# Kernel tuning notes

Hardware: AMD Instinct MI355X
Metric: run time of the kernel (lower is better)

## Reference

```python
import jax, jax.numpy as jnp
import numpy as np

B, N, OBS_DIM = 64, 512, 128
HIDDEN_DIM, MESSAGE_DIM, ACTION_DIM = 256, 128, 16


def _dense_params(key, din, dout):
    kw, kb = jax.random.split(key)
    W = jax.random.normal(kw, (din, dout), jnp.float32) * 0.02
    b = jnp.zeros((dout,), jnp.float32)
    return W, b


def setup_inputs() -> dict:
    key = jax.random.key(0)
    ks = jax.random.split(key, 12)
    obs_batch = jax.random.normal(ks[0], (B, N, OBS_DIM), jnp.float32)
    dones_batch = jnp.zeros((B, N), jnp.bool_)
    We, be = _dense_params(ks[1], OBS_DIM, HIDDEN_DIM)
    Wc, bc = _dense_params(ks[2], HIDDEN_DIM, MESSAGE_DIM // 4)
    Wn, bn = _dense_params(ks[3], HIDDEN_DIM, MESSAGE_DIM // 2)
    Wb, bb = _dense_params(ks[4], HIDDEN_DIM, MESSAGE_DIM // 4)
    Wi, bi = _dense_params(ks[5], HIDDEN_DIM, 1)
    Wq, bq = _dense_params(ks[6], HIDDEN_DIM, MESSAGE_DIM)
    Wk, bk = _dense_params(ks[7], MESSAGE_DIM, MESSAGE_DIM)
    Wv, bv = _dense_params(ks[8], MESSAGE_DIM, MESSAGE_DIM)
    Wp, bp = _dense_params(ks[9], HIDDEN_DIM + MESSAGE_DIM, HIDDEN_DIM)
    Wa, ba = _dense_params(ks[10], HIDDEN_DIM, ACTION_DIM)
    Wcr, bcr = _dense_params(ks[11], HIDDEN_DIM, 1)
    return {"obs_batch": obs_batch, "dones_batch": dones_batch,
            "We": We, "be": be, "Wc": Wc, "bc": bc, "Wn": Wn, "bn": bn,
            "Wb": Wb, "bb": bb, "Wi": Wi, "bi": bi, "Wq": Wq, "bq": bq,
            "Wk": Wk, "bk": bk, "Wv": Wv, "bv": bv, "Wp": Wp, "bp": bp,
            "Wa": Wa, "ba": ba, "Wcr": Wcr, "bcr": bcr}


def reference(obs_batch, dones_batch, We, be, Wc, bc, Wn, bn, Wb, bb, Wi, bi,
              Wq, bq, Wk, bk, Wv, bv, Wp, bp, Wa, ba, Wcr, bcr):
    dense = lambda x, W, b: x @ W + b
    encoded = jax.nn.relu(dense(obs_batch, We, be))                 # [B,N,H]
    messages = jnp.concatenate([dense(encoded, Wc, bc),
                                dense(encoded, Wn, bn),
                                dense(encoded, Wb, bb)], axis=-1)   # [B,N,M]
    importance = jax.nn.sigmoid(dense(encoded, Wi, bi))             # [B,N,1]
    Q = dense(encoded, Wq, bq)
    K = dense(messages, Wk, bk)
    V = dense(messages, Wv, bv)
    scores = jnp.einsum('bqd,bkd->bqk', Q, K) / jnp.sqrt(jnp.float32(MESSAGE_DIM))
    importance_weights = importance * jnp.transpose(importance, (0, 2, 1))  # [B,N,N]
    scores = scores * importance_weights
    norms = jnp.linalg.norm(obs_batch, axis=-1, keepdims=True)      # [B,N,1]
    obs_sim = jnp.einsum('bid,bjd->bij', obs_batch, obs_batch)
    obs_sim = obs_sim / (norms + 1e-08)
    obs_sim = obs_sim / (jnp.transpose(norms, (0, 2, 1)) + 1e-08)
    scores = scores + obs_sim * 0.5
    attn = jax.nn.softmax(scores, axis=-1)
    aggregated = jnp.einsum('bqk,bkd->bqd', attn, V)                # [B,N,M]
    combined = jnp.concatenate([encoded, aggregated], axis=-1)
    x = jax.nn.relu(dense(combined, Wp, bp))
    logits = dense(x, Wa, ba)
    value = dense(x, Wcr, bcr).squeeze(-1)
    return (logits, value)
```

## Files before the change

### kernel.cpp

```cpp
#include <hip/hip_runtime.h>
#include <math.h>


typedef __attribute__((ext_vector_type(8))) short short8;
typedef __attribute__((ext_vector_type(4))) float f32x4;

#define RSQRT_D 0.08838834764831843f

__device__ __forceinline__ unsigned short f2bf(float f) {
  union { float f; unsigned u; } v; v.f = f;
  return (unsigned short)((v.u + 0x7FFFu + ((v.u >> 16) & 1u)) >> 16);
}
__device__ __forceinline__ float bf2f(unsigned short h) {
  union { unsigned u; float f; } v; v.u = ((unsigned)h) << 16;
  return v.f;
}
__device__ __forceinline__ unsigned pack2(float a, float b) {
  return (unsigned)f2bf(a) | ((unsigned)f2bf(b) << 16);
}

__device__ __forceinline__ int swz(int row, int chunk) {
  return row * 128 + ((chunk ^ ((row & 7) << 1)) << 3);
}

__global__ __launch_bounds__(256) void prep_w(
    const float* __restrict__ We, const float* __restrict__ Wq,
    const float* __restrict__ Wk, const float* __restrict__ Wv,
    const float* __restrict__ Wp, const float* __restrict__ Wc,
    const float* __restrict__ Wn, const float* __restrict__ Wb,
    const float* __restrict__ bc, const float* __restrict__ bn,
    const float* __restrict__ bb, const float* __restrict__ Wa,
    const float* __restrict__ Wcr, unsigned short* __restrict__ WeT,
    unsigned short* __restrict__ Wmq, unsigned short* __restrict__ Wkv,
    unsigned short* __restrict__ WpT, unsigned short* __restrict__ WaCrT,
    float* __restrict__ bm) {
  int idx = blockIdx.x * 256 + threadIdx.x;
  if (idx < 32768) {
    int n = idx >> 7, k = idx & 127;
    WeT[idx] = f2bf(We[k * 256 + n]);
  } else if (idx < 65536) {
    int i = idx - 32768;
    int d = i >> 8, h = i & 255;
    float v = (d < 32)   ? Wc[h * 32 + d]
            : (d < 96)   ? Wn[h * 64 + (d - 32)]
                         : Wb[h * 32 + (d - 96)];
    Wmq[i] = f2bf(v);
  } else if (idx < 98304) {
    int i = idx - 65536;
    int n = i >> 8, k = i & 255;
    Wmq[32768 + i] = f2bf(Wq[k * 128 + n]);
  } else if (idx < 114688) {
    int i = idx - 98304;
    int n = i >> 7, k = i & 127;
    Wkv[i] = f2bf(Wk[k * 128 + n]);
  } else if (idx < 131072) {
    int i = idx - 114688;
    int n = i >> 7, k = i & 127;
    Wkv[16384 + i] = f2bf(Wv[k * 128 + n]);
  } else if (idx < 229376) {
    int i = idx - 131072;
    int n = i / 384, k = i - n * 384;
    WpT[i] = f2bf(Wp[k * 256 + n]);
  } else if (idx < 237568) {
    int i = idx - 229376;
    int n = i >> 8, k = i & 255;
    float v = (n < 16) ? Wa[k * 16 + n] : (n == 16) ? Wcr[k] : 0.f;
    WaCrT[i] = f2bf(v);
  } else if (idx < 237696) {
    int i = idx - 237568;
    bm[i] = (i < 32) ? bc[i] : (i < 96) ? bn[i - 32] : bb[i - 96];
  }
}

__global__ __launch_bounds__(256) void prep_obs(
    const float* __restrict__ obs, unsigned short* __restrict__ obs_bf,
    unsigned short* __restrict__ As, unsigned short* __restrict__ Bs) {
  int t = blockIdx.x * 4 + (threadIdx.x >> 6);
  int lane = threadIdx.x & 63;
  const float* row = obs + (size_t)t * 128;
  float2 o = *(const float2*)(row + lane * 2);
  float s2 = o.x * o.x + o.y * o.y;
#pragma unroll
  for (int off = 1; off < 64; off <<= 1) s2 += __shfl_xor(s2, off);
  float inv = 1.f / (sqrtf(s2) + 1e-8f);
  ((unsigned*)obs_bf)[(size_t)t * 64 + lane] = pack2(o.x, o.y);
  ((unsigned*)As)[(size_t)t * 128 + 64 + lane] =
      pack2(o.x * 0.5f * inv, o.y * 0.5f * inv);
  ((unsigned*)Bs)[(size_t)t * 128 + 64 + lane] = pack2(o.x * inv, o.y * inv);
}

__global__ __launch_bounds__(256) void imp_kernel(
    const unsigned short* __restrict__ enc, const float* __restrict__ Wi,
    const float* __restrict__ bi, float* __restrict__ impA,
    float* __restrict__ impB) {
  int t = blockIdx.x * 4 + (threadIdx.x >> 6);
  int lane = threadIdx.x & 63;
  const unsigned* eu = (const unsigned*)(enc + (size_t)t * 256);
  unsigned u0 = eu[lane * 2], u1 = eu[lane * 2 + 1];
  float4 w = *(const float4*)(Wi + lane * 4);
  float s = bf2f((unsigned short)(u0 & 0xFFFF)) * w.x +
            bf2f((unsigned short)(u0 >> 16)) * w.y +
            bf2f((unsigned short)(u1 & 0xFFFF)) * w.z +
            bf2f((unsigned short)(u1 >> 16)) * w.w;
#pragma unroll
  for (int off = 1; off < 64; off <<= 1) s += __shfl_xor(s, off);
  if (lane == 0) {
    float sg = 1.0f / (1.0f + __expf(-(s + bi[0])));
    impA[t] = sg * RSQRT_D;
    impB[t] = sg;
  }
}

template <int MODE>
__device__ __forceinline__ void epi_store(unsigned short* out, int ldc,
                                          const float* bias,
                                          const float* scale, int rowb,
                                          int col, const f32x4& a) {
  const float bv = bias ? bias[col] : 0.f;
  if constexpr (MODE == 3) {
    unsigned short t0 = f2bf(a[0] + bv), t1 = f2bf(a[1] + bv);
    unsigned short t2 = f2bf(a[2] + bv), t3 = f2bf(a[3] + bv);
    uint2 o;
    o.x = (unsigned)t0 | ((unsigned)t1 << 16);
    o.y = (unsigned)t2 | ((unsigned)t3 << 16);
    *(uint2*)(out + ((size_t)(rowb >> 9) * 128 + col) * 512 + (rowb & 511)) = o;
  } else {
#pragma unroll
    for (int r = 0; r < 4; ++r) {
      float v = a[r] + bv;
      if constexpr (MODE == 1) v = fmaxf(v, 0.f);
      if constexpr (MODE == 2) v *= scale[rowb + r];
      out[(size_t)(rowb + r) * ldc + col] = f2bf(v);
    }
  }
}

template <int M0, int M1>
__global__ __launch_bounds__(256, 2) void gemm_dual(
    const unsigned short* __restrict__ A1, int lda1, int K1,
    const unsigned short* __restrict__ A2, int lda2, int Ktot,
    const unsigned short* __restrict__ Bt, int ldb,
    const float* __restrict__ bias0, const float* __restrict__ bias1,
    const float* __restrict__ scale, unsigned short* __restrict__ out0,
    int ldc0, unsigned short* __restrict__ out1, int ldc1, int xsplit) {
  __shared__ unsigned short Asr[64][72];
  __shared__ unsigned short Bsr[128][72];
  const int tid = threadIdx.x;
  const int lane = tid & 63, wave = tid >> 6;
  const int quad = lane >> 4, l16 = lane & 15;
  const int wm = wave & 1, wn = wave >> 1;
  const int bm = blockIdx.y * 64, bn = blockIdx.x * 128;

  f32x4 acc[2][4];
#pragma unroll
  for (int i = 0; i < 2; ++i)
#pragma unroll
    for (int j = 0; j < 4; ++j) acc[i][j] = (f32x4){0.f, 0.f, 0.f, 0.f};

  const int ar = tid >> 3, ac = tid & 7;
  for (int kt = 0; kt < Ktot; kt += 64) {
    const unsigned short* Asrc;
    int lda, kloc;
    if (kt < K1) { Asrc = A1; lda = lda1; kloc = kt; }
    else         { Asrc = A2; lda = lda2; kloc = kt - K1; }
#pragma unroll
    for (int it = 0; it < 2; ++it) {
      int r = ar + it * 32;
      uint4 v = *(const uint4*)(Asrc + (size_t)(bm + r) * lda + kloc + ac * 8);
      *(uint4*)&Asr[r][ac * 8] = v;
    }
#pragma unroll
    for (int it = 0; it < 4; ++it) {
      int r = ar + it * 32;
      uint4 v = *(const uint4*)(Bt + (size_t)(bn + r) * ldb + kt + ac * 8);
      *(uint4*)&Bsr[r][ac * 8] = v;
    }
    __syncthreads();
#pragma unroll
    for (int ks = 0; ks < 64; ks += 32) {
      short8 af[2], bfr[4];
#pragma unroll
      for (int i = 0; i < 2; ++i)
        af[i] = *(const short8*)&Asr[wm * 32 + i * 16 + l16][ks + quad * 8];
#pragma unroll
      for (int j = 0; j < 4; ++j)
        bfr[j] = *(const short8*)&Bsr[wn * 64 + j * 16 + l16][ks + quad * 8];
#pragma unroll
      for (int i = 0; i < 2; ++i)
#pragma unroll
        for (int j = 0; j < 4; ++j)
          acc[i][j] = __builtin_amdgcn_mfma_f32_16x16x32_bf16(af[i], bfr[j],
                                                              acc[i][j], 0, 0, 0);
    }
    __syncthreads();
  }
  const int colb = bn + wn * 64 + l16;
#pragma unroll
  for (int i = 0; i < 2; ++i) {
    const int rowb = bm + wm * 32 + i * 16 + quad * 4;
#pragma unroll
    for (int j = 0; j < 4; ++j) {
      const int col = colb + j * 16;
      if (col < xsplit)
        epi_store<M0>(out0, ldc0, bias0, scale, rowb, col, acc[i][j]);
      else
        epi_store<M1>(out1, ldc1, bias1, scale, rowb, col - xsplit, acc[i][j]);
    }
  }
}

__global__ __launch_bounds__(256, 3) void flash2(
    const unsigned short* __restrict__ As, const unsigned short* __restrict__ Bs,
    const unsigned short* __restrict__ vT, unsigned short* __restrict__ agg) {
  __shared__ unsigned short Ub[128 * 128];
  __shared__ unsigned short Pp[32 * 128];
  __shared__ float redm[2][32];
  __shared__ float reds[2][32];
  const int tid = threadIdx.x;
  const int lane = tid & 63, wave = tid >> 6;
  const int quad = lane >> 4, l16 = lane & 15;
  const int wm = wave & 1, wn = wave >> 1;
  const int b = blockIdx.x & 63;
  const int qt = blockIdx.x >> 6;
  const size_t tokA = (size_t)b * 512 + qt * 32;

  short8 af[8];
#pragma unroll
  for (int kc = 0; kc < 8; ++kc)
    af[kc] = *(const short8*)(As + (tokA + wm * 16 + l16) * 256 + kc * 32 +
                              quad * 8);

  f32x4 s[4][4];
#pragma unroll
  for (int kt = 0; kt < 4; ++kt)
#pragma unroll
    for (int nt = 0; nt < 4; ++nt) s[kt][nt] = (f32x4){0.f, 0.f, 0.f, 0.f};

  const int lr = tid >> 4, lc = tid & 15;

#pragma unroll
  for (int kt = 0; kt < 4; ++kt) {
#pragma unroll
    for (int kh = 0; kh < 2; ++kh) {
      __syncthreads();
#pragma unroll
      for (int it = 0; it < 8; ++it) {
        int r = lr + it * 16;
        *(uint4*)&Ub[swz(r, lc)] =
            *(const uint4*)(Bs + ((size_t)b * 512 + kt * 128 + r) * 256 +
                            kh * 128 + lc * 8);
      }
      __syncthreads();
#pragma unroll
      for (int kk = 0; kk < 4; ++kk) {
        short8 bfr[4];
#pragma unroll
        for (int nt = 0; nt < 4; ++nt) {
          int rrow = wn * 64 + nt * 16 + l16;
          bfr[nt] = *(const short8*)&Ub[swz(rrow, kk * 4 + quad)];
        }
#pragma unroll
        for (int nt = 0; nt < 4; ++nt)
          s[kt][nt] = __builtin_amdgcn_mfma_f32_16x16x32_bf16(
              af[kh * 4 + kk], bfr[nt], s[kt][nt], 0, 0, 0);
      }
    }
  }

  const int rbase = wm * 16 + quad * 4;
  float mt4[4];
#pragma unroll
  for (int r = 0; r < 4; ++r) {
    float mv = -1e30f;
#pragma unroll
    for (int kt = 0; kt < 4; ++kt)
#pragma unroll
      for (int nt = 0; nt < 4; ++nt) mv = fmaxf(mv, s[kt][nt][r]);
#pragma unroll
    for (int off = 1; off < 16; off <<= 1) mv = fmaxf(mv, __shfl_xor(mv, off));
    mt4[r] = mv;
  }
  if (l16 == 0) {
#pragma unroll
    for (int r = 0; r < 4; ++r) redm[wn][rbase + r] = mt4[r];
  }
  __syncthreads();
  float lsum[4];
#pragma unroll
  for (int r = 0; r < 4; ++r) {
    float mfull = fmaxf(mt4[r], redm[1 ^ wn][rbase + r]);
    float sum = 0.f;
#pragma unroll
    for (int kt = 0; kt < 4; ++kt)
#pragma unroll
      for (int nt = 0; nt < 4; ++nt) {
        float p = __expf(s[kt][nt][r] - mfull);
        s[kt][nt][r] = p;
        sum += p;
      }
#pragma unroll
    for (int off = 1; off < 16; off <<= 1) sum += __shfl_xor(sum, off);
    lsum[r] = sum;
  }
  if (l16 == 0) {
#pragma unroll
    for (int r = 0; r < 4; ++r) reds[wn][rbase + r] = lsum[r];
  }
  __syncthreads();
  float linv[4];
#pragma unroll
  for (int r = 0; r < 4; ++r)
    linv[r] = 1.0f / (lsum[r] + reds[1 ^ wn][rbase + r]);

  f32x4 oacc[4];
#pragma unroll
  for (int nt = 0; nt < 4; ++nt) oacc[nt] = (f32x4){0.f, 0.f, 0.f, 0.f};
#pragma unroll
  for (int vt = 0; vt < 4; ++vt) {
    __syncthreads();
#pragma unroll
    for (int nt = 0; nt < 4; ++nt)
#pragma unroll
      for (int r = 0; r < 4; ++r) {
        int row = rbase + r;
        int col = wn * 64 + nt * 16 + l16;
        Pp[row * 128 + (((col >> 3) ^ ((row & 7) << 1)) << 3) + (col & 7)] =
            f2bf(s[vt][nt][r]);
      }
#pragma unroll
    for (int it = 0; it < 8; ++it) {
      int r = lr + it * 16;
      *(uint4*)&Ub[swz(r, lc)] =
          *(const uint4*)(vT + ((size_t)b * 128 + r) * 512 + vt * 128 + lc * 8);
    }
    __syncthreads();
#pragma unroll
    for (int kk = 0; kk < 4; ++kk) {
      short8 pa = *(const short8*)&Pp[swz(wm * 16 + l16, kk * 4 + quad)];
#pragma unroll
      for (int nt = 0; nt < 4; ++nt) {
        int rrow = wn * 64 + nt * 16 + l16;
        short8 vb = *(const short8*)&Ub[swz(rrow, kk * 4 + quad)];
        oacc[nt] = __builtin_amdgcn_mfma_f32_16x16x32_bf16(pa, vb, oacc[nt],
                                                           0, 0, 0);
      }
    }
  }

#pragma unroll
  for (int nt = 0; nt < 4; ++nt) {
    const int col = wn * 64 + nt * 16 + l16;
#pragma unroll
    for (int r = 0; r < 4; ++r)
      agg[(tokA + rbase + r) * 128 + col] = f2bf(oacc[nt][r] * linv[r]);
  }
}

__global__ __launch_bounds__(256, 3) void xh_gemm(
    const unsigned short* __restrict__ A1, const unsigned short* __restrict__ A2,
    const unsigned short* __restrict__ WpT, const float* __restrict__ bp,
    const unsigned short* __restrict__ WaCrT, const float* __restrict__ ba,
    const float* __restrict__ bcr, float* __restrict__ logits,
    float* __restrict__ value) {
  __shared__ unsigned short Asr[32][72];
  __shared__ unsigned short Bsr[256][72];
  const int tid = threadIdx.x;
  const int lane = tid & 63, wave = tid >> 6;
  const int quad = lane >> 4, l16 = lane & 15;
  const int bm = blockIdx.x * 32;

  f32x4 acc[2][4];
#pragma unroll
  for (int i = 0; i < 2; ++i)
#pragma unroll
    for (int j = 0; j < 4; ++j) acc[i][j] = (f32x4){0.f, 0.f, 0.f, 0.f};

  const int ar = tid >> 3, ac = tid & 7;
  for (int kt = 0; kt < 384; kt += 64) {
    const unsigned short* Asrc;
    int lda, kloc;
    if (kt < 256) { Asrc = A1; lda = 256; kloc = kt; }
    else          { Asrc = A2; lda = 128; kloc = kt - 256; }
    *(uint4*)&Asr[ar][ac * 8] =
        *(const uint4*)(Asrc + (size_t)(bm + ar) * lda + kloc + ac * 8);
#pragma unroll
    for (int it = 0; it < 8; ++it) {
      int idx = tid + it * 256;
      int r = idx >> 3, c = idx & 7;
      *(uint4*)&Bsr[r][c * 8] = *(const uint4*)(WpT + (size_t)r * 384 + kt + c * 8);
    }
    __syncthreads();
#pragma unroll
    for (int kk = 0; kk < 2; ++kk) {
      short8 afr[2], bfr[4];
#pragma unroll
      for (int i = 0; i < 2; ++i)
        afr[i] = *(const short8*)&Asr[i * 16 + l16][kk * 32 + quad * 8];
#pragma unroll
      for (int j = 0; j < 4; ++j)
        bfr[j] = *(const short8*)&Bsr[wave * 64 + j * 16 + l16][kk * 32 + quad * 8];
#pragma unroll
      for (int i = 0; i < 2; ++i)
#pragma unroll
        for (int j = 0; j < 4; ++j)
          acc[i][j] = __builtin_amdgcn_mfma_f32_16x16x32_bf16(afr[i], bfr[j],
                                                              acc[i][j], 0, 0, 0);
    }
    __syncthreads();
  }
  unsigned short* xs = &Bsr[0][0];
#pragma unroll
  for (int i = 0; i < 2; ++i) {
    const int row = i * 16 + quad * 4;
#pragma unroll
    for (int j = 0; j < 4; ++j) {
      const int col = wave * 64 + j * 16 + l16;
      const float bv = bp[col];
#pragma unroll
      for (int r = 0; r < 4; ++r)
        xs[(row + r) * 264 + col] = f2bf(fmaxf(acc[i][j][r] + bv, 0.f));
    }
  }
  __syncthreads();
  const int wm2 = wave & 1, wn2 = wave >> 1;
  f32x4 hacc = (f32x4){0.f, 0.f, 0.f, 0.f};
#pragma unroll
  for (int kk = 0; kk < 8; ++kk) {
    short8 pa = *(const short8*)&xs[(wm2 * 16 + l16) * 264 + kk * 32 + quad * 8];
    short8 wb = *(const short8*)(WaCrT + (size_t)(wn2 * 16 + l16) * 256 +
                                 kk * 32 + quad * 8);
    hacc = __builtin_amdgcn_mfma_f32_16x16x32_bf16(pa, wb, hacc, 0, 0, 0);
  }
  const int n = wn2 * 16 + l16;
#pragma unroll
  for (int r = 0; r < 4; ++r) {
    const size_t tok = bm + wm2 * 16 + quad * 4 + r;
    if (n < 16)
      logits[tok * 16 + n] = hacc[r] + ba[n];
    else if (n == 16)
      value[tok] = hacc[r] + bcr[0];
  }
}

extern "C" void kernel_launch(void* const* d_in, const int* in_sizes, int n_in,
                              void* d_out, int out_size, void* d_ws,
                              size_t ws_size, hipStream_t stream) {
  const float* obs = (const float*)d_in[0];
  const float* We = (const float*)d_in[2];
  const float* be = (const float*)d_in[3];
  const float* Wc = (const float*)d_in[4];
  const float* bc = (const float*)d_in[5];
  const float* Wn = (const float*)d_in[6];
  const float* bn = (const float*)d_in[7];
  const float* Wb = (const float*)d_in[8];
  const float* bb = (const float*)d_in[9];
  const float* Wi = (const float*)d_in[10];
  const float* bi = (const float*)d_in[11];
  const float* Wq = (const float*)d_in[12];
  const float* bq = (const float*)d_in[13];
  const float* Wk = (const float*)d_in[14];
  const float* bk = (const float*)d_in[15];
  const float* Wv = (const float*)d_in[16];
  const float* bv = (const float*)d_in[17];
  const float* Wp = (const float*)d_in[18];
  const float* bp = (const float*)d_in[19];
  const float* Wa = (const float*)d_in[20];
  const float* ba = (const float*)d_in[21];
  const float* Wcr = (const float*)d_in[22];
  const float* bcr = (const float*)d_in[23];

  char* base = (char*)d_ws;
  unsigned short* enc_bf = (unsigned short*)(base);
  unsigned short* As     = (unsigned short*)(base + 16777216);
  unsigned short* Bs     = (unsigned short*)(base + 33554432);
  unsigned short* obsagg = (unsigned short*)(base + 50331648);
  unsigned short* msg_bf = (unsigned short*)(base + 58720256);
  unsigned short* vT     = (unsigned short*)(base + 75497472);
  float* impA            = (float*)(base + 83886080);
  float* impB            = (float*)(base + 84017152);
  unsigned short* WeT    = (unsigned short*)(base + 84148224);
  unsigned short* Wmq    = (unsigned short*)(base + 84213760);
  unsigned short* Wkv    = (unsigned short*)(base + 84344832);
  unsigned short* WpT    = (unsigned short*)(base + 84410368);
  float* bmb             = (float*)(base + 84606976);
  unsigned short* WaCrT  = (unsigned short*)(base + 84607488);

  prep_w<<<929, 256, 0, stream>>>(We, Wq, Wk, Wv, Wp, Wc, Wn, Wb, bc, bn, bb,
                                  Wa, Wcr, WeT, Wmq, Wkv, WpT, WaCrT, bmb);
  prep_obs<<<8192, 256, 0, stream>>>(obs, obsagg, As, Bs);

  gemm_dual<1, 1><<<dim3(2, 512), 256, 0, stream>>>(
      obsagg, 128, 128, nullptr, 0, 128, WeT, 128, be, be, nullptr, enc_bf,
      256, enc_bf, 256, 256);
  imp_kernel<<<8192, 256, 0, stream>>>(enc_bf, Wi, bi, impA, impB);

  gemm_dual<0, 2><<<dim3(2, 512), 256, 0, stream>>>(
      enc_bf, 256, 256, nullptr, 0, 256, Wmq, 256, bmb, bq, impA, msg_bf, 128,
      As, 256, 128);
  gemm_dual<2, 3><<<dim3(2, 512), 256, 0, stream>>>(
      msg_bf, 128, 128, nullptr, 0, 128, Wkv, 128, bk, bv, impB, Bs, 256, vT,
      0, 128);

  flash2<<<1024, 256, 0, stream>>>(As, Bs, vT, obsagg);

  xh_gemm<<<1024, 256, 0, stream>>>(enc_bf, obsagg, WpT, bp, WaCrT, ba, bcr,
                                    (float*)d_out, (float*)d_out + 524288);
}
```

Baseline: 223.2 us.

## Replace LDS-staged GEMMs with direct-load MFMA kernels and fuse importance into encoder

Every GEMM kernel now loads MFMA fragments straight from global memory instead of staging tiles through shared memory with barriers. The importance projection and sigmoid move into the encoder GEMM epilogue, which removes a separate kernel and a re-read of the encoded activations. The attention kernel is restructured so each wave owns a 128-key slice, with a four-way cross-wave max and sum reduction and the whole P tile kept in LDS. The trade-off is more redundant global and L2 traffic from unshared fragment loads, and the loss of the LDS swizzling.

```diff
diff --git a/kernel.cpp b/kernel.cpp
--- a/kernel.cpp
+++ b/kernel.cpp
@@ -6,6 +6,7 @@
 typedef __attribute__((ext_vector_type(4))) float f32x4;
 
 #define RSQRT_D 0.08838834764831843f
+#define MFMA __builtin_amdgcn_mfma_f32_16x16x32_bf16
 
 __device__ __forceinline__ unsigned short f2bf(float f) {
   union { float f; unsigned u; } v; v.f = f;
@@ -18,9 +19,8 @@
 __device__ __forceinline__ unsigned pack2(float a, float b) {
   return (unsigned)f2bf(a) | ((unsigned)f2bf(b) << 16);
 }
-
-__device__ __forceinline__ int swz(int row, int chunk) {
-  return row * 128 + ((chunk ^ ((row & 7) << 1)) << 3);
+__device__ __forceinline__ short8 ld8(const unsigned short* p) {
+  return *(const short8*)p;
 }
 
 __global__ __launch_bounds__(256) void prep_w(
@@ -89,336 +89,351 @@
   ((unsigned*)Bs)[(size_t)t * 128 + 64 + lane] = pack2(o.x * inv, o.y * inv);
 }
 
-__global__ __launch_bounds__(256) void imp_kernel(
-    const unsigned short* __restrict__ enc, const float* __restrict__ Wi,
-    const float* __restrict__ bi, float* __restrict__ impA,
+__global__ __launch_bounds__(256) void enc_gemm(
+    const unsigned short* __restrict__ obs_bf,
+    const unsigned short* __restrict__ WeT, const float* __restrict__ be,
+    const float* __restrict__ Wi, const float* __restrict__ bi,
+    unsigned short* __restrict__ enc, float* __restrict__ impA,
     float* __restrict__ impB) {
-  int t = blockIdx.x * 4 + (threadIdx.x >> 6);
-  int lane = threadIdx.x & 63;
-  const unsigned* eu = (const unsigned*)(enc + (size_t)t * 256);
-  unsigned u0 = eu[lane * 2], u1 = eu[lane * 2 + 1];
-  float4 w = *(const float4*)(Wi + lane * 4);
-  float s = bf2f((unsigned short)(u0 & 0xFFFF)) * w.x +
-            bf2f((unsigned short)(u0 >> 16)) * w.y +
-            bf2f((unsigned short)(u1 & 0xFFFF)) * w.z +
-            bf2f((unsigned short)(u1 >> 16)) * w.w;
-#pragma unroll
-  for (int off = 1; off < 64; off <<= 1) s += __shfl_xor(s, off);
-  if (lane == 0) {
-    float sg = 1.0f / (1.0f + __expf(-(s + bi[0])));
-    impA[t] = sg * RSQRT_D;
-    impB[t] = sg;
-  }
-}
-
-template <int MODE>
-__device__ __forceinline__ void epi_store(unsigned short* out, int ldc,
-                                          const float* bias,
-                                          const float* scale, int rowb,
-                                          int col, const f32x4& a) {
-  const float bv = bias ? bias[col] : 0.f;
-  if constexpr (MODE == 3) {
-    unsigned short t0 = f2bf(a[0] + bv), t1 = f2bf(a[1] + bv);
-    unsigned short t2 = f2bf(a[2] + bv), t3 = f2bf(a[3] + bv);
-    uint2 o;
-    o.x = (unsigned)t0 | ((unsigned)t1 << 16);
-    o.y = (unsigned)t2 | ((unsigned)t3 << 16);
-    *(uint2*)(out + ((size_t)(rowb >> 9) * 128 + col) * 512 + (rowb & 511)) = o;
-  } else {
+  __shared__ float ired[4][32];
+  const int tid = threadIdx.x, lane = tid & 63, wave = tid >> 6;
+  const int quad = lane >> 4, l16 = lane & 15;
+  const int bm = blockIdx.x * 32;
+  f32x4 acc[2][4];
+#pragma unroll
+  for (int i = 0; i < 2; ++i)
+#pragma unroll
+    for (int j = 0; j < 4; ++j) acc[i][j] = (f32x4){0.f, 0.f, 0.f, 0.f};
+#pragma unroll
+  for (int kc = 0; kc < 4; ++kc) {
+    short8 af[2], bf[4];
+#pragma unroll
+    for (int i = 0; i < 2; ++i)
+      af[i] = ld8(obs_bf + (size_t)(bm + i * 16 + l16) * 128 + kc * 32 + quad * 8);
+#pragma unroll
+    for (int j = 0; j < 4; ++j)
+      bf[j] = ld8(WeT + (size_t)(wave * 64 + j * 16 + l16) * 128 + kc * 32 + quad * 8);
+#pragma unroll
+    for (int i = 0; i < 2; ++i)
+#pragma unroll
+      for (int j = 0; j < 4; ++j) acc[i][j] = MFMA(af[i], bf[j], acc[i][j], 0, 0, 0);
+  }
+  float ip[2][4];
+#pragma unroll
+  for (int i = 0; i < 2; ++i)
+#pragma unroll
+    for (int r = 0; r < 4; ++r) ip[i][r] = 0.f;
+#pragma unroll
+  for (int i = 0; i < 2; ++i)
+#pragma unroll
+    for (int j = 0; j < 4; ++j) {
+      const int col = wave * 64 + j * 16 + l16;
+      const float bv = be[col], wv = Wi[col];
+      const int rowb = bm + i * 16 + quad * 4;
+#pragma unroll
+      for (int r = 0; r < 4; ++r) {
+        float v = fmaxf(acc[i][j][r] + bv, 0.f);
+        enc[(size_t)(rowb + r) * 256 + col] = f2bf(v);
+        ip[i][r] += v * wv;
+      }
+    }
+#pragma unroll
+  for (int i = 0; i < 2; ++i)
 #pragma unroll
     for (int r = 0; r < 4; ++r) {
-      float v = a[r] + bv;
-      if constexpr (MODE == 1) v = fmaxf(v, 0.f);
-      if constexpr (MODE == 2) v *= scale[rowb + r];
-      out[(size_t)(rowb + r) * ldc + col] = f2bf(v);
-    }
-  }
-}
-
-template <int M0, int M1>
-__global__ __launch_bounds__(256, 2) void gemm_dual(
-    const unsigned short* __restrict__ A1, int lda1, int K1,
-    const unsigned short* __restrict__ A2, int lda2, int Ktot,
-    const unsigned short* __restrict__ Bt, int ldb,
-    const float* __restrict__ bias0, const float* __restrict__ bias1,
-    const float* __restrict__ scale, unsigned short* __restrict__ out0,
-    int ldc0, unsigned short* __restrict__ out1, int ldc1, int xsplit) {
-  __shared__ unsigned short Asr[64][72];
-  __shared__ unsigned short Bsr[128][72];
-  const int tid = threadIdx.x;
-  const int lane = tid & 63, wave = tid >> 6;
+#pragma unroll
+      for (int off = 1; off < 16; off <<= 1)
+        ip[i][r] += __shfl_xor(ip[i][r], off);
+    }
+  if (l16 == 0) {
+#pragma unroll
+    for (int i = 0; i < 2; ++i)
+#pragma unroll
+      for (int r = 0; r < 4; ++r)
+        ired[wave][i * 16 + quad * 4 + r] = ip[i][r];
+  }
+  __syncthreads();
+  if (tid < 32) {
+    float s = ired[0][tid] + ired[1][tid] + ired[2][tid] + ired[3][tid] + bi[0];
+    float sg = 1.0f / (1.0f + __expf(-s));
+    impA[bm + tid] = sg * RSQRT_D;
+    impB[bm + tid] = sg;
+  }
+}
+
+__global__ __launch_bounds__(256) void msgq_gemm(
+    const unsigned short* __restrict__ enc, const unsigned short* __restrict__ Wmq,
+    const float* __restrict__ bm, const float* __restrict__ bq,
+    const float* __restrict__ impA, unsigned short* __restrict__ msg,
+    unsigned short* __restrict__ As) {
+  const int tid = threadIdx.x, lane = tid & 63, wave = tid >> 6;
   const int quad = lane >> 4, l16 = lane & 15;
-  const int wm = wave & 1, wn = wave >> 1;
-  const int bm = blockIdx.y * 64, bn = blockIdx.x * 128;
-
+  const int bmr = blockIdx.x * 32;
   f32x4 acc[2][4];
 #pragma unroll
   for (int i = 0; i < 2; ++i)
 #pragma unroll
     for (int j = 0; j < 4; ++j) acc[i][j] = (f32x4){0.f, 0.f, 0.f, 0.f};
-
-  const int ar = tid >> 3, ac = tid & 7;
-  for (int kt = 0; kt < Ktot; kt += 64) {
-    const unsigned short* Asrc;
-    int lda, kloc;
-    if (kt < K1) { Asrc = A1; lda = lda1; kloc = kt; }
-    else         { Asrc = A2; lda = lda2; kloc = kt - K1; }
-#pragma unroll
-    for (int it = 0; it < 2; ++it) {
-      int r = ar + it * 32;
-      uint4 v = *(const uint4*)(Asrc + (size_t)(bm + r) * lda + kloc + ac * 8);
-      *(uint4*)&Asr[r][ac * 8] = v;
-    }
-#pragma unroll
-    for (int it = 0; it < 4; ++it) {
-      int r = ar + it * 32;
-      uint4 v = *(const uint4*)(Bt + (size_t)(bn + r) * ldb + kt + ac * 8);
-      *(uint4*)&Bsr[r][ac * 8] = v;
-    }
-    __syncthreads();
-#pragma unroll
-    for (int ks = 0; ks < 64; ks += 32) {
-      short8 af[2], bfr[4];
-#pragma unroll
-      for (int i = 0; i < 2; ++i)
-        af[i] = *(const short8*)&Asr[wm * 32 + i * 16 + l16][ks + quad * 8];
-#pragma unroll
-      for (int j = 0; j < 4; ++j)
-        bfr[j] = *(const short8*)&Bsr[wn * 64 + j * 16 + l16][ks + quad * 8];
-#pragma unroll
-      for (int i = 0; i < 2; ++i)
-#pragma unroll
-        for (int j = 0; j < 4; ++j)
-          acc[i][j] = __builtin_amdgcn_mfma_f32_16x16x32_bf16(af[i], bfr[j],
-                                                              acc[i][j], 0, 0, 0);
-    }
-    __syncthreads();
-  }
-  const int colb = bn + wn * 64 + l16;
+#pragma unroll
+  for (int kc = 0; kc < 8; ++kc) {
+    short8 af[2], bf[4];
+#pragma unroll
+    for (int i = 0; i < 2; ++i)
+      af[i] = ld8(enc + (size_t)(bmr + i * 16 + l16) * 256 + kc * 32 + quad * 8);
+#pragma unroll
+    for (int j = 0; j < 4; ++j)
+      bf[j] = ld8(Wmq + (size_t)(wave * 64 + j * 16 + l16) * 256 + kc * 32 + quad * 8);
+#pragma unroll
+    for (int i = 0; i < 2; ++i)
+#pragma unroll
+      for (int j = 0; j < 4; ++j) acc[i][j] = MFMA(af[i], bf[j], acc[i][j], 0, 0, 0);
+  }
 #pragma unroll
   for (int i = 0; i < 2; ++i) {
-    const int rowb = bm + wm * 32 + i * 16 + quad * 4;
+    const int rowb = bmr + i * 16 + quad * 4;
 #pragma unroll
     for (int j = 0; j < 4; ++j) {
-      const int col = colb + j * 16;
-      if (col < xsplit)
-        epi_store<M0>(out0, ldc0, bias0, scale, rowb, col, acc[i][j]);
-      else
-        epi_store<M1>(out1, ldc1, bias1, scale, rowb, col - xsplit, acc[i][j]);
-    }
-  }
-}
-
-__global__ __launch_bounds__(256, 3) void flash2(
+      const int col = wave * 64 + j * 16 + l16;
+      if (col < 128) {
+        const float bv = bm[col];
+#pragma unroll
+        for (int r = 0; r < 4; ++r)
+          msg[(size_t)(rowb + r) * 128 + col] = f2bf(acc[i][j][r] + bv);
+      } else {
+        const int c = col - 128;
+        const float bv = bq[c];
+#pragma unroll
+        for (int r = 0; r < 4; ++r)
+          As[(size_t)(rowb + r) * 256 + c] =
+              f2bf((acc[i][j][r] + bv) * impA[rowb + r]);
+      }
+    }
+  }
+}
+
+__global__ __launch_bounds__(256) void kv_gemm(
+    const unsigned short* __restrict__ msg, const unsigned short* __restrict__ Wkv,
+    const float* __restrict__ bk, const float* __restrict__ bv,
+    const float* __restrict__ impB, unsigned short* __restrict__ Bs,
+    unsigned short* __restrict__ vT) {
+  const int tid = threadIdx.x, lane = tid & 63, wave = tid >> 6;
+  const int quad = lane >> 4, l16 = lane & 15;
+  const int bmr = blockIdx.x * 32;
+  f32x4 acc[2][4];
+#pragma unroll
+  for (int i = 0; i < 2; ++i)
+#pragma unroll
+    for (int j = 0; j < 4; ++j) acc[i][j] = (f32x4){0.f, 0.f, 0.f, 0.f};
+#pragma unroll
+  for (int kc = 0; kc < 4; ++kc) {
+    short8 af[2], bf[4];
+#pragma unroll
+    for (int i = 0; i < 2; ++i)
+      af[i] = ld8(msg + (size_t)(bmr + i * 16 + l16) * 128 + kc * 32 + quad * 8);
+#pragma unroll
+    for (int j = 0; j < 4; ++j)
+      bf[j] = ld8(Wkv + (size_t)(wave * 64 + j * 16 + l16) * 128 + kc * 32 + quad * 8);
+#pragma unroll
+    for (int i = 0; i < 2; ++i)
+#pragma unroll
+      for (int j = 0; j < 4; ++j) acc[i][j] = MFMA(af[i], bf[j], acc[i][j], 0, 0, 0);
+  }
+#pragma unroll
+  for (int i = 0; i < 2; ++i) {
+    const int rowb = bmr + i * 16 + quad * 4;
+#pragma unroll
+    for (int j = 0; j < 4; ++j) {
+      const int col = wave * 64 + j * 16 + l16;
+      if (col < 128) {
+        const float bvv = bk[col];
+#pragma unroll
+        for (int r = 0; r < 4; ++r)
+          Bs[(size_t)(rowb + r) * 256 + col] =
+              f2bf((acc[i][j][r] + bvv) * impB[rowb + r]);
+      } else {
+        const int c = col - 128;
+        const float bvv = bv[c];
+        uint2 o;
+        o.x = pack2(acc[i][j][0] + bvv, acc[i][j][1] + bvv);
+        o.y = pack2(acc[i][j][2] + bvv, acc[i][j][3] + bvv);
+        *(uint2*)(vT + ((size_t)(rowb >> 9) * 128 + c) * 512 + (rowb & 511)) = o;
+      }
+    }
+  }
+}
+
+__global__ __launch_bounds__(256) void flash3(
     const unsigned short* __restrict__ As, const unsigned short* __restrict__ Bs,
     const unsigned short* __restrict__ vT, unsigned short* __restrict__ agg) {
-  __shared__ unsigned short Ub[128 * 128];
-  __shared__ unsigned short Pp[32 * 128];
-  __shared__ float redm[2][32];
-  __shared__ float reds[2][32];
-  const int tid = threadIdx.x;
-  const int lane = tid & 63, wave = tid >> 6;
+  __shared__ unsigned short Pp[32 * 520];
+  __shared__ float redm[4][32];
+  __shared__ float reds[4][32];
+  const int tid = threadIdx.x, lane = tid & 63, wave = tid >> 6;
   const int quad = lane >> 4, l16 = lane & 15;
-  const int wm = wave & 1, wn = wave >> 1;
   const int b = blockIdx.x & 63;
   const int qt = blockIdx.x >> 6;
-  const size_t tokA = (size_t)b * 512 + qt * 32;
-
-  short8 af[8];
-#pragma unroll
-  for (int kc = 0; kc < 8; ++kc)
-    af[kc] = *(const short8*)(As + (tokA + wm * 16 + l16) * 256 + kc * 32 +
-                              quad * 8);
-
-  f32x4 s[4][4];
-#pragma unroll
-  for (int kt = 0; kt < 4; ++kt)
-#pragma unroll
-    for (int nt = 0; nt < 4; ++nt) s[kt][nt] = (f32x4){0.f, 0.f, 0.f, 0.f};
-
-  const int lr = tid >> 4, lc = tid & 15;
-
-#pragma unroll
-  for (int kt = 0; kt < 4; ++kt) {
-#pragma unroll
-    for (int kh = 0; kh < 2; ++kh) {
-      __syncthreads();
-#pragma unroll
-      for (int it = 0; it < 8; ++it) {
-        int r = lr + it * 16;
-        *(uint4*)&Ub[swz(r, lc)] =
-            *(const uint4*)(Bs + ((size_t)b * 512 + kt * 128 + r) * 256 +
-                            kh * 128 + lc * 8);
-      }
-      __syncthreads();
-#pragma unroll
-      for (int kk = 0; kk < 4; ++kk) {
-        short8 bfr[4];
-#pragma unroll
-        for (int nt = 0; nt < 4; ++nt) {
-          int rrow = wn * 64 + nt * 16 + l16;
-          bfr[nt] = *(const short8*)&Ub[swz(rrow, kk * 4 + quad)];
-        }
-#pragma unroll
-        for (int nt = 0; nt < 4; ++nt)
-          s[kt][nt] = __builtin_amdgcn_mfma_f32_16x16x32_bf16(
-              af[kh * 4 + kk], bfr[nt], s[kt][nt], 0, 0, 0);
-      }
-    }
-  }
-
-  const int rbase = wm * 16 + quad * 4;
-  float mt4[4];
-#pragma unroll
-  for (int r = 0; r < 4; ++r) {
-    float mv = -1e30f;
-#pragma unroll
-    for (int kt = 0; kt < 4; ++kt)
-#pragma unroll
-      for (int nt = 0; nt < 4; ++nt) mv = fmaxf(mv, s[kt][nt][r]);
-#pragma unroll
-    for (int off = 1; off < 16; off <<= 1) mv = fmaxf(mv, __shfl_xor(mv, off));
-    mt4[r] = mv;
-  }
+  const size_t tok0 = (size_t)b * 512 + qt * 32;
+
+  f32x4 s[2][8];
+#pragma unroll
+  for (int i = 0; i < 2; ++i)
+#pragma unroll
+    for (int nt = 0; nt < 8; ++nt) s[i][nt] = (f32x4){0.f, 0.f, 0.f, 0.f};
+
+#pragma unroll
+  for (int kc = 0; kc < 8; ++kc) {
+    short8 af[2];
+#pragma unroll
+    for (int i = 0; i < 2; ++i)
+      af[i] = ld8(As + (tok0 + i * 16 + l16) * 256 + kc * 32 + quad * 8);
+#pragma unroll
+    for (int nt = 0; nt < 8; ++nt) {
+      short8 bf = ld8(Bs + ((size_t)b * 512 + wave * 128 + nt * 16 + l16) * 256 +
+                      kc * 32 + quad * 8);
+#pragma unroll
+      for (int i = 0; i < 2; ++i) s[i][nt] = MFMA(af[i], bf, s[i][nt], 0, 0, 0);
+    }
+  }
+
+  float mt[2][4];
+#pragma unroll
+  for (int i = 0; i < 2; ++i)
+#pragma unroll
+    for (int r = 0; r < 4; ++r) {
+      float mv = -1e30f;
+#pragma unroll
+      for (int nt = 0; nt < 8; ++nt) mv = fmaxf(mv, s[i][nt][r]);
+#pragma unroll
+      for (int off = 1; off < 16; off <<= 1) mv = fmaxf(mv, __shfl_xor(mv, off));
+      mt[i][r] = mv;
+    }
   if (l16 == 0) {
 #pragma unroll
-    for (int r = 0; r < 4; ++r) redm[wn][rbase + r] = mt4[r];
+    for (int i = 0; i < 2; ++i)
+#pragma unroll
+      for (int r = 0; r < 4; ++r) redm[wave][i * 16 + quad * 4 + r] = mt[i][r];
   }
   __syncthreads();
-  float lsum[4];
-#pragma unroll
-  for (int r = 0; r < 4; ++r) {
-    float mfull = fmaxf(mt4[r], redm[1 ^ wn][rbase + r]);
-    float sum = 0.f;
-#pragma unroll
-    for (int kt = 0; kt < 4; ++kt)
-#pragma unroll
-      for (int nt = 0; nt < 4; ++nt) {
-        float p = __expf(s[kt][nt][r] - mfull);
-        s[kt][nt][r] = p;
+  float lsum[2][4];
+#pragma unroll
+  for (int i = 0; i < 2; ++i)
+#pragma unroll
+    for (int r = 0; r < 4; ++r) {
+      const int row = i * 16 + quad * 4 + r;
+      float mfull = fmaxf(fmaxf(redm[0][row], redm[1][row]),
+                          fmaxf(redm[2][row], redm[3][row]));
+      float sum = 0.f;
+#pragma unroll
+      for (int nt = 0; nt < 8; ++nt) {
+        float p = __expf(s[i][nt][r] - mfull);
+        s[i][nt][r] = p;
         sum += p;
       }
 #pragma unroll
-    for (int off = 1; off < 16; off <<= 1) sum += __shfl_xor(sum, off);
-    lsum[r] = sum;
-  }
+      for (int off = 1; off < 16; off <<= 1) sum += __shfl_xor(sum, off);
+      lsum[i][r] = sum;
+    }
   if (l16 == 0) {
 #pragma unroll
-    for (int r = 0; r < 4; ++r) reds[wn][rbase + r] = lsum[r];
-  }
+    for (int i = 0; i < 2; ++i)
+#pragma unroll
+      for (int r = 0; r < 4; ++r) reds[wave][i * 16 + quad * 4 + r] = lsum[i][r];
+  }
+#pragma unroll
+  for (int i = 0; i < 2; ++i)
+#pragma unroll
+    for (int nt = 0; nt < 8; ++nt) {
+      const int col = wave * 128 + nt * 16 + l16;
+#pragma unroll
+      for (int r = 0; r < 4; ++r)
+        Pp[(i * 16 + quad * 4 + r) * 520 + col] = f2bf(s[i][nt][r]);
+    }
   __syncthreads();
-  float linv[4];
-#pragma unroll
-  for (int r = 0; r < 4; ++r)
-    linv[r] = 1.0f / (lsum[r] + reds[1 ^ wn][rbase + r]);
-
-  f32x4 oacc[4];
-#pragma unroll
-  for (int nt = 0; nt < 4; ++nt) oacc[nt] = (f32x4){0.f, 0.f, 0.f, 0.f};
-#pragma unroll
-  for (int vt = 0; vt < 4; ++vt) {
-    __syncthreads();
-#pragma unroll
-    for (int nt = 0; nt < 4; ++nt)
-#pragma unroll
-      for (int r = 0; r < 4; ++r) {
-        int row = rbase + r;
-        int col = wn * 64 + nt * 16 + l16;
-        Pp[row * 128 + (((col >> 3) ^ ((row & 7) << 1)) << 3) + (col & 7)] =
-            f2bf(s[vt][nt][r]);
-      }
-#pragma unroll
-    for (int it = 0; it < 8; ++it) {
-      int r = lr + it * 16;
-      *(uint4*)&Ub[swz(r, lc)] =
-          *(const uint4*)(vT + ((size_t)b * 128 + r) * 512 + vt * 128 + lc * 8);
-    }
-    __syncthreads();
-#pragma unroll
-    for (int kk = 0; kk < 4; ++kk) {
-      short8 pa = *(const short8*)&Pp[swz(wm * 16 + l16, kk * 4 + quad)];
-#pragma unroll
-      for (int nt = 0; nt < 4; ++nt) {
-        int rrow = wn * 64 + nt * 16 + l16;
-        short8 vb = *(const short8*)&Ub[swz(rrow, kk * 4 + quad)];
-        oacc[nt] = __builtin_amdgcn_mfma_f32_16x16x32_bf16(pa, vb, oacc[nt],
-                                                           0, 0, 0);
-      }
-    }
-  }
-
-#pragma unroll
-  for (int nt = 0; nt < 4; ++nt) {
-    const int col = wn * 64 + nt * 16 + l16;
-#pragma unroll
-    for (int r = 0; r < 4; ++r)
-      agg[(tokA + rbase + r) * 128 + col] = f2bf(oacc[nt][r] * linv[r]);
-  }
-}
-
-__global__ __launch_bounds__(256, 3) void xh_gemm(
-    const unsigned short* __restrict__ A1, const unsigned short* __restrict__ A2,
+  float linv[2][4];
+#pragma unroll
+  for (int i = 0; i < 2; ++i)
+#pragma unroll
+    for (int r = 0; r < 4; ++r) {
+      const int row = i * 16 + quad * 4 + r;
+      linv[i][r] =
+          1.0f / (reds[0][row] + reds[1][row] + reds[2][row] + reds[3][row]);
+    }
+
+  f32x4 o[2][2];
+#pragma unroll
+  for (int i = 0; i < 2; ++i)
+#pragma unroll
+    for (int j = 0; j < 2; ++j) o[i][j] = (f32x4){0.f, 0.f, 0.f, 0.f};
+#pragma unroll
+  for (int kc = 0; kc < 16; ++kc) {
+    short8 pa[2];
+#pragma unroll
+    for (int i = 0; i < 2; ++i)
+      pa[i] = *(const short8*)&Pp[(i * 16 + l16) * 520 + kc * 32 + quad * 8];
+#pragma unroll
+    for (int j = 0; j < 2; ++j) {
+      short8 vb = ld8(vT + ((size_t)b * 128 + wave * 32 + j * 16 + l16) * 512 +
+                      kc * 32 + quad * 8);
+#pragma unroll
+      for (int i = 0; i < 2; ++i) o[i][j] = MFMA(pa[i], vb, o[i][j], 0, 0, 0);
+    }
+  }
+#pragma unroll
+  for (int i = 0; i < 2; ++i) {
+    const size_t rowb = tok0 + i * 16 + quad * 4;
+#pragma unroll
+    for (int j = 0; j < 2; ++j) {
+      const int col = wave * 32 + j * 16 + l16;
+#pragma unroll
+      for (int r = 0; r < 4; ++r)
+        agg[(rowb + r) * 128 + col] = f2bf(o[i][j][r] * linv[i][r]);
+    }
+  }
+}
+
+__global__ __launch_bounds__(256) void xh_gemm(
+    const unsigned short* __restrict__ enc, const unsigned short* __restrict__ agg,
     const unsigned short* __restrict__ WpT, const float* __restrict__ bp,
     const unsigned short* __restrict__ WaCrT, const float* __restrict__ ba,
     const float* __restrict__ bcr, float* __restrict__ logits,
     float* __restrict__ value) {
-  __shared__ unsigned short Asr[32][72];
-  __shared__ unsigned short Bsr[256][72];
-  const int tid = threadIdx.x;
-  const int lane = tid & 63, wave = tid >> 6;
+  __shared__ unsigned short xs[32][264];
+  const int tid = threadIdx.x, lane = tid & 63, wave = tid >> 6;
   const int quad = lane >> 4, l16 = lane & 15;
   const int bm = blockIdx.x * 32;
-
   f32x4 acc[2][4];
 #pragma unroll
   for (int i = 0; i < 2; ++i)
 #pragma unroll
     for (int j = 0; j < 4; ++j) acc[i][j] = (f32x4){0.f, 0.f, 0.f, 0.f};
-
-  const int ar = tid >> 3, ac = tid & 7;
-  for (int kt = 0; kt < 384; kt += 64) {
-    const unsigned short* Asrc;
-    int lda, kloc;
-    if (kt < 256) { Asrc = A1; lda = 256; kloc = kt; }
-    else          { Asrc = A2; lda = 128; kloc = kt - 256; }
-    *(uint4*)&Asr[ar][ac * 8] =
-        *(const uint4*)(Asrc + (size_t)(bm + ar) * lda + kloc + ac * 8);
-#pragma unroll
-    for (int it = 0; it < 8; ++it) {
-      int idx = tid + it * 256;
-      int r = idx >> 3, c = idx & 7;
-      *(uint4*)&Bsr[r][c * 8] = *(const uint4*)(WpT + (size_t)r * 384 + kt + c * 8);
-    }
-    __syncthreads();
-#pragma unroll
-    for (int kk = 0; kk < 2; ++kk) {
-      short8 afr[2], bfr[4];
-#pragma unroll
-      for (int i = 0; i < 2; ++i)
-        afr[i] = *(const short8*)&Asr[i * 16 + l16][kk * 32 + quad * 8];
-#pragma unroll
-      for (int j = 0; j < 4; ++j)
-        bfr[j] = *(const short8*)&Bsr[wave * 64 + j * 16 + l16][kk * 32 + quad * 8];
-#pragma unroll
-      for (int i = 0; i < 2; ++i)
-#pragma unroll
-        for (int j = 0; j < 4; ++j)
-          acc[i][j] = __builtin_amdgcn_mfma_f32_16x16x32_bf16(afr[i], bfr[j],
-                                                              acc[i][j], 0, 0, 0);
-    }
-    __syncthreads();
-  }
-  unsigned short* xs = &Bsr[0][0];
+#pragma unroll
+  for (int kc = 0; kc < 12; ++kc) {
+    const unsigned short* A;
+    int lda, ko;
+    if (kc < 8) { A = enc; lda = 256; ko = kc * 32; }
+    else        { A = agg; lda = 128; ko = (kc - 8) * 32; }
+    short8 af[2], bf[4];
+#pragma unroll
+    for (int i = 0; i < 2; ++i)
+      af[i] = ld8(A + (size_t)(bm + i * 16 + l16) * lda + ko + quad * 8);
+#pragma unroll
+    for (int j = 0; j < 4; ++j)
+      bf[j] = ld8(WpT + (size_t)(wave * 64 + j * 16 + l16) * 384 + kc * 32 + quad * 8);
+#pragma unroll
+    for (int i = 0; i < 2; ++i)
+#pragma unroll
+      for (int j = 0; j < 4; ++j) acc[i][j] = MFMA(af[i], bf[j], acc[i][j], 0, 0, 0);
+  }
 #pragma unroll
   for (int i = 0; i < 2; ++i) {
     const int row = i * 16 + quad * 4;
 #pragma unroll
     for (int j = 0; j < 4; ++j) {
       const int col = wave * 64 + j * 16 + l16;
-      const float bv = bp[col];
+      const float bvv = bp[col];
 #pragma unroll
       for (int r = 0; r < 4; ++r)
-        xs[(row + r) * 264 + col] = f2bf(fmaxf(acc[i][j][r] + bv, 0.f));
+        xs[row + r][col] = f2bf(fmaxf(acc[i][j][r] + bvv, 0.f));
     }
   }
   __syncthreads();
@@ -426,10 +441,9 @@
   f32x4 hacc = (f32x4){0.f, 0.f, 0.f, 0.f};
 #pragma unroll
   for (int kk = 0; kk < 8; ++kk) {
-    short8 pa = *(const short8*)&xs[(wm2 * 16 + l16) * 264 + kk * 32 + quad * 8];
-    short8 wb = *(const short8*)(WaCrT + (size_t)(wn2 * 16 + l16) * 256 +
-                                 kk * 32 + quad * 8);
-    hacc = __builtin_amdgcn_mfma_f32_16x16x32_bf16(pa, wb, hacc, 0, 0, 0);
+    short8 pa = *(const short8*)&xs[wm2 * 16 + l16][kk * 32 + quad * 8];
+    short8 wb = ld8(WaCrT + (size_t)(wn2 * 16 + l16) * 256 + kk * 32 + quad * 8);
+    hacc = MFMA(pa, wb, hacc, 0, 0, 0);
   }
   const int n = wn2 * 16 + l16;
 #pragma unroll
@@ -489,20 +503,11 @@
                                   Wa, Wcr, WeT, Wmq, Wkv, WpT, WaCrT, bmb);
   prep_obs<<<8192, 256, 0, stream>>>(obs, obsagg, As, Bs);
 
-  gemm_dual<1, 1><<<dim3(2, 512), 256, 0, stream>>>(
-      obsagg, 128, 128, nullptr, 0, 128, WeT, 128, be, be, nullptr, enc_bf,
-      256, enc_bf, 256, 256);
-  imp_kernel<<<8192, 256, 0, stream>>>(enc_bf, Wi, bi, impA, impB);
-
-  gemm_dual<0, 2><<<dim3(2, 512), 256, 0, stream>>>(
-      enc_bf, 256, 256, nullptr, 0, 256, Wmq, 256, bmb, bq, impA, msg_bf, 128,
-      As, 256, 128);
-  gemm_dual<2, 3><<<dim3(2, 512), 256, 0, stream>>>(
-      msg_bf, 128, 128, nullptr, 0, 128, Wkv, 128, bk, bv, impB, Bs, 256, vT,
-      0, 128);
-
-  flash2<<<1024, 256, 0, stream>>>(As, Bs, vT, obsagg);
-
+  enc_gemm<<<1024, 256, 0, stream>>>(obsagg, WeT, be, Wi, bi, enc_bf, impA,
+                                     impB);
+  msgq_gemm<<<1024, 256, 0, stream>>>(enc_bf, Wmq, bmb, bq, impA, msg_bf, As);
+  kv_gemm<<<1024, 256, 0, stream>>>(msg_bf, Wkv, bk, bv, impB, Bs, vT);
+  flash3<<<1024, 256, 0, stream>>>(As, Bs, vT, obsagg);
   xh_gemm<<<1024, 256, 0, stream>>>(enc_bf, obsagg, WpT, bp, WaCrT, ba, bcr,
                                     (float*)d_out, (float*)d_out + 524288);
 }
```

New measurement: 278.9 us. 24.9% more time.
